# Kernel optimization log

Measured on AMD Instinct MI355X. Metric: run time of the kernel, lower is better.

Reference implementation:

```python
import jax, jax.numpy as jnp
import numpy as np

B, L, D, N = 1, 4096, 1536, 12
d = D // N            # head_dim = 128
c = d // 2            # rope channels per head = 64
EPS = 1e-6
MAX_POS = 1024


def setup_inputs() -> dict:
    key = jax.random.key(0)
    ks = jax.random.split(key, 8)
    s = 0.02
    # RoPE tables: freqs[m, j] = m * theta^{-j/c}; torch stores exp(i*ang) as complex64
    inv = 1.0 / (10000.0 ** (jnp.arange(c, dtype=jnp.float32) / c))
    ang = jnp.arange(MAX_POS, dtype=jnp.float32)[:, None] * inv[None, :]
    return {
        'x': jax.random.normal(ks[0], (B, L, D), jnp.float32),
        'seq_lens': jnp.array([L], jnp.int32),
        'grid_sizes': jnp.array([[4, 32, 32]], jnp.int32),  # f*h*w == L
        'freqs_cos': jnp.cos(ang),
        'freqs_sin': jnp.sin(ang),
        'Wq': jax.random.normal(ks[1], (D, D), jnp.float32) * s,
        'bq': jnp.zeros((D,), jnp.float32),
        'Wk': jax.random.normal(ks[2], (D, D), jnp.float32) * s,
        'bk': jnp.zeros((D,), jnp.float32),
        'Wv': jax.random.normal(ks[3], (D, D), jnp.float32) * s,
        'bv': jnp.zeros((D,), jnp.float32),
        'Wo': jax.random.normal(ks[4], (D, D), jnp.float32) * s,
        'bo': jnp.zeros((D,), jnp.float32),
        'gq': jnp.ones((D,), jnp.float32),
        'gk': jnp.ones((D,), jnp.float32),
    }


def rms_norm(x, g):
    # WanRMSNorm over the full model dim, computed in fp32
    v = jnp.mean(x.astype(jnp.float32) ** 2, axis=-1, keepdims=True)
    return (x * jax.lax.rsqrt(v + EPS)).astype(x.dtype) * g


def rope_apply(x4, grid_sizes, fcos, fsin):
    # x4: [B, L, N, d]; grid_sizes: [B, 3]; applies 3D (f,h,w) RoPE per batch
    gs = np.asarray(grid_sizes)  # concrete grid sizes (structural constants)
    c1 = c - 2 * (c // 3)
    c2 = c // 3
    outs = []
    for i in range(x4.shape[0]):
        f, h, w = (int(gs[i, 0]), int(gs[i, 1]), int(gs[i, 2]))
        sl = f * h * w

        def grid(tab):
            a = jnp.broadcast_to(tab[:f, None, None, :c1], (f, h, w, c1))
            b = jnp.broadcast_to(tab[None, :h, None, c1:c1 + c2], (f, h, w, c2))
            cc = jnp.broadcast_to(tab[None, None, :w, c1 + c2:c], (f, h, w, c2))
            return jnp.concatenate([a, b, cc], axis=-1).reshape(sl, 1, c)

        cos_i, sin_i = grid(fcos), grid(fsin)
        xi = x4[i, :sl]                    # [sl, N, d]
        xr, xim = xi[..., 0::2], xi[..., 1::2]  # complex pairs are interleaved
        o_re = xr * cos_i - xim * sin_i
        o_im = xr * sin_i + xim * cos_i
        rot = jnp.stack([o_re, o_im], axis=-1).reshape(sl, x4.shape[2], d)
        outs.append(jnp.concatenate([rot, x4[i, sl:]], axis=0))
    return jnp.stack(outs).astype(x4.dtype)


def reference(x, seq_lens, grid_sizes, freqs_cos, freqs_sin,
              Wq, bq, Wk, bk, Wv, bv, Wo, bo, gq, gk):
    q = rms_norm(x @ Wq.T + bq, gq).reshape(B, L, N, d)
    k = rms_norm(x @ Wk.T + bk, gk).reshape(B, L, N, d)
    v = (x @ Wv.T + bv).reshape(B, L, N, d)
    q = rope_apply(q, grid_sizes, freqs_cos, freqs_sin)
    k = rope_apply(k, grid_sizes, freqs_cos, freqs_sin)
    scale = 1.0 / jnp.sqrt(jnp.float32(d))
    scores = jnp.einsum('bqnd,bknd->bnqk', q, k) * scale
    kmask = jnp.arange(L)[None, :] < seq_lens[:, None]        # [B, L]
    scores = jnp.where(kmask[:, None, None, :], scores, jnp.float32(-1e30))
    p = jax.nn.softmax(scores, axis=-1)
    out = jnp.einsum('bnqk,bknd->bqnd', p, v).reshape(B, L, D)
    return out @ Wo.T + bo
```

## Files before the change

kernel.cpp:

```cpp
#include <hip/hip_runtime.h>

#define L_ 4096
#define D_ 1536
#define NH 12
#define HD 128

typedef __attribute__((ext_vector_type(8))) __bf16 bf16x8;
typedef __attribute__((ext_vector_type(8))) unsigned short ushort8v;
typedef __attribute__((ext_vector_type(4))) float floatx4;

#if __has_builtin(__builtin_amdgcn_exp2f)
#define EXP2F(x) __builtin_amdgcn_exp2f(x)
#else
#define EXP2F(x) exp2f(x)
#endif

__device__ __forceinline__ unsigned short f2bf(float f) {
  union { float f; unsigned int u; } v; v.f = f;
  unsigned int u = v.u;
  return (unsigned short)((u + 0x7fffu + ((u >> 16) & 1u)) >> 16);
}
__device__ __forceinline__ float bf2f(unsigned short h) {
  union { unsigned int u; float f; } v; v.u = ((unsigned int)h) << 16;
  return v.f;
}

__global__ __launch_bounds__(256) void cvt_f32_bf16(const float* __restrict__ in,
                                                    unsigned short* __restrict__ out,
                                                    int n8) {
  int i = blockIdx.x * 256 + threadIdx.x;
  if (i >= n8) return;
  const float4* p = (const float4*)(in + (size_t)i * 8);
  float4 a = p[0], b = p[1];
  ushort8v o;
  o[0] = f2bf(a.x); o[1] = f2bf(a.y); o[2] = f2bf(a.z); o[3] = f2bf(a.w);
  o[4] = f2bf(b.x); o[5] = f2bf(b.y); o[6] = f2bf(b.z); o[7] = f2bf(b.w);
  *(ushort8v*)(out + (size_t)i * 8) = o;
}

template <int MODE>
__device__ __forceinline__ void gemm_core(const unsigned short* __restrict__ A,
                                          const unsigned short* __restrict__ Bw,
                                          const float* __restrict__ bias,
                                          void* __restrict__ Cout,
                                          int M, int Nn, int K,
                                          int m0, int n0,
                                          unsigned short* As, unsigned short* Bs) {
  int t = threadIdx.x;
  int lane = t & 63, wv = t >> 6;
  int wm = (wv & 1) * 64, wn = (wv >> 1) * 64;
  floatx4 zero = {0.f, 0.f, 0.f, 0.f};
  floatx4 acc[4][4];
#pragma unroll
  for (int i = 0; i < 4; ++i)
#pragma unroll
    for (int j = 0; j < 4; ++j) acc[i][j] = zero;
  int fm = lane & 15, fk = (lane >> 4) * 8;

  for (int kt = 0; kt < K; kt += 32) {
    __syncthreads();
#pragma unroll
    for (int it = 0; it < 2; ++it) {
      int c = it * 256 + t;
      int row = c >> 2, col = (c & 3) * 8;
      const unsigned short* ga = A + (size_t)(m0 + row) * K + kt + col;
      const unsigned short* gb = Bw + (size_t)(n0 + row) * K + kt + col;
      __builtin_amdgcn_global_load_lds(
          (const __attribute__((address_space(1))) void*)ga,
          (__attribute__((address_space(3))) void*)((char*)As + (it * 256 + wv * 64) * 16),
          16, 0, 0);
      __builtin_amdgcn_global_load_lds(
          (const __attribute__((address_space(1))) void*)gb,
          (__attribute__((address_space(3))) void*)((char*)Bs + (it * 256 + wv * 64) * 16),
          16, 0, 0);
    }
    __syncthreads();
    bf16x8 af[4], bfr[4];
#pragma unroll
    for (int i = 0; i < 4; ++i) {
      af[i]  = *(const bf16x8*)&As[(wm + 16 * i + fm) * 32 + fk];
      bfr[i] = *(const bf16x8*)&Bs[(wn + 16 * i + fm) * 32 + fk];
    }
#pragma unroll
    for (int i = 0; i < 4; ++i)
#pragma unroll
      for (int j = 0; j < 4; ++j)
        acc[i][j] = __builtin_amdgcn_mfma_f32_16x16x32_bf16(af[i], bfr[j], acc[i][j], 0, 0, 0);
  }

  int fr = (lane >> 4) * 4;
#pragma unroll
  for (int j = 0; j < 4; ++j) {
    int col = n0 + wn + 16 * j + fm;
    float bz = bias[col];
#pragma unroll
    for (int i = 0; i < 4; ++i) {
      int row0 = m0 + wm + 16 * i + fr;
      if (MODE == 2) {
        ushort4 pk = make_ushort4(f2bf(acc[i][j][0] + bz), f2bf(acc[i][j][1] + bz),
                                  f2bf(acc[i][j][2] + bz), f2bf(acc[i][j][3] + bz));
        size_t off = (size_t)(row0 >> 5) * Nn * 32 + (size_t)col * 32 + (row0 & 31);
        *(ushort4*)&((unsigned short*)Cout)[off] = pk;
      } else {
#pragma unroll
        for (int r = 0; r < 4; ++r) {
          float val = acc[i][j][r] + bz;
          if (MODE == 1) ((unsigned short*)Cout)[(size_t)(row0 + r) * Nn + col] = f2bf(val);
          else           ((float*)Cout)[(size_t)(row0 + r) * Nn + col] = val;
        }
      }
    }
  }
}

template <int MODE>
__global__ __launch_bounds__(256) void gemm_bt(const unsigned short* __restrict__ A,
                                               const unsigned short* __restrict__ Bw,
                                               const float* __restrict__ bias,
                                               void* __restrict__ Cout,
                                               int M, int Nn, int K) {
  __shared__ unsigned short As[128 * 32];
  __shared__ unsigned short Bs[128 * 32];
  gemm_core<MODE>(A, Bw, bias, Cout, M, Nn, K, blockIdx.y * 128, blockIdx.x * 128, As, Bs);
}

__global__ __launch_bounds__(256) void gemm_qkv(const unsigned short* __restrict__ xb,
                                                const unsigned short* __restrict__ wq,
                                                const unsigned short* __restrict__ wk,
                                                const unsigned short* __restrict__ wv,
                                                const float* __restrict__ bq,
                                                const float* __restrict__ bk,
                                                const float* __restrict__ bv,
                                                unsigned short* __restrict__ outq,
                                                unsigned short* __restrict__ outk,
                                                unsigned short* __restrict__ outv) {
  __shared__ unsigned short As[128 * 32];
  __shared__ unsigned short Bs[128 * 32];
  int which = blockIdx.x / (D_ / 128);
  int n0 = (blockIdx.x % (D_ / 128)) * 128;
  int m0 = blockIdx.y * 128;
  if (which == 0)
    gemm_core<1>(xb, wq, bq, outq, L_, D_, D_, m0, n0, As, Bs);
  else if (which == 1)
    gemm_core<1>(xb, wk, bk, outk, L_, D_, D_, m0, n0, As, Bs);
  else
    gemm_core<2>(xb, wv, bv, outv, L_, D_, D_, m0, n0, As, Bs);
}

__global__ __launch_bounds__(256) void rmsrope(unsigned short* __restrict__ qb,
                                               unsigned short* __restrict__ kb,
                                               const float* __restrict__ gq,
                                               const float* __restrict__ gk,
                                               const float* __restrict__ fcos,
                                               const float* __restrict__ fsin,
                                               const int* __restrict__ grid_sizes) {
  int row = blockIdx.x;
  unsigned short* buf = (blockIdx.y == 0) ? qb : kb;
  const float* g = (blockIdx.y == 0) ? gq : gk;
  float osc = (blockIdx.y == 0) ? 0.1275174475f : 1.0f;
  int t = threadIdx.x;
  float xr[3], xi[3];
#pragma unroll
  for (int i = 0; i < 3; ++i) {
    int p = t + i * 256;
    unsigned int raw = *(const unsigned int*)&buf[(size_t)row * D_ + 2 * p];
    xr[i] = bf2f((unsigned short)(raw & 0xffffu));
    xi[i] = bf2f((unsigned short)(raw >> 16));
  }
  float ss = 0.f;
#pragma unroll
  for (int i = 0; i < 3; ++i) ss += xr[i] * xr[i] + xi[i] * xi[i];
  for (int off = 32; off > 0; off >>= 1) ss += __shfl_down(ss, off);
  __shared__ float red[4];
  if ((t & 63) == 0) red[t >> 6] = ss;
  __syncthreads();
  float rs = rsqrtf((red[0] + red[1] + red[2] + red[3]) * (1.0f / D_) + 1e-6f);

  int gf = grid_sizes[0], gh = grid_sizes[1], gw = grid_sizes[2];
  int sl = gf * gh * gw;
  int hw = gh * gw;
  int fi = row / hw, rem = row - fi * hw;
  int hi = rem / gw, wi = rem - hi * gw;
  bool dorope = row < sl;
#pragma unroll
  for (int i = 0; i < 3; ++i) {
    int p = t + i * 256;
    int j = p & 63;
    float a = xr[i] * rs * g[2 * p];
    float b = xi[i] * rs * g[2 * p + 1];
    if (dorope) {
      int pos = (j < 22) ? fi : ((j < 43) ? hi : wi);
      float cs = fcos[pos * 64 + j], sn = fsin[pos * 64 + j];
      float oa = a * cs - b * sn;
      float ob = a * sn + b * cs;
      a = oa; b = ob;
    }
    a *= osc; b *= osc;
    unsigned int packed = (unsigned int)f2bf(a) | ((unsigned int)f2bf(b) << 16);
    *(unsigned int*)&buf[(size_t)row * D_ + 2 * p] = packed;
  }
}

__global__ __launch_bounds__(256, 2) void attn7(const unsigned short* __restrict__ Qb,
                                                const unsigned short* __restrict__ Kb,
                                                const unsigned short* __restrict__ Vt,
                                                float* __restrict__ Op0,
                                                float* __restrict__ Op1,
                                                float* __restrict__ lp,
                                                const int* __restrict__ seq_lens) {
  __shared__ unsigned short Ks[2][4096];
  __shared__ unsigned short Vs[2][4096];
  int t = threadIdx.x, lane = t & 63, w = t >> 6;
  int id = blockIdx.x;
  int u2 = (id & 7) * 96 + (id >> 3);
  int half = u2 & 1, v = u2 >> 1;
  int h = v >> 5, qt = v & 31;
  int q0 = qt * 128 + w * 32;
  int kv0 = half * 2048;
  float* Opart = half ? Op1 : Op0;
  float* lpart = lp + (size_t)half * L_ * NH;
  int seqlen = seq_lens[0];
  int fl = lane & 15, fg = lane >> 4;

  bf16x8 qf[2][4];
#pragma unroll
  for (int nj = 0; nj < 2; ++nj)
#pragma unroll
    for (int kd = 0; kd < 4; ++kd)
      qf[nj][kd] = *(const bf16x8*)&Qb[((size_t)(q0 + nj * 16 + fl) * NH + h) * HD + kd * 32 + fg * 8];

  const unsigned short* kp[2];
  const unsigned short* vp[2];
#pragma unroll
  for (int i = 0; i < 2; ++i) {
    int c = t + i * 256;
    int dgroup = c >> 5, permrow = c & 31;
    int kd = dgroup >> 2, fgc = dgroup & 3, mi = permrow >> 4, flc = permrow & 15;
    int key = (((flc & 12) << 1) | (flc & 3)) + (mi << 2);
    kp[i] = Kb + ((size_t)(kv0 + key) * NH + h) * HD + kd * 32 + fgc * 8;
    int vd = c & 127, vkg = c >> 7;
    vp[i] = Vt + (size_t)(kv0 >> 5) * (D_ * 32) + ((size_t)(h * HD + vd)) * 32 + vkg * 8;
  }
  const int STEP = 32 * NH * HD;

  auto stage = [&](int b) {
#pragma unroll
    for (int i = 0; i < 2; ++i) {
      __builtin_amdgcn_global_load_lds(
          (const __attribute__((address_space(1))) void*)kp[i],
          (__attribute__((address_space(3))) void*)&Ks[b][(i * 256 + w * 64) * 8],
          16, 0, 0);
      __builtin_amdgcn_global_load_lds(
          (const __attribute__((address_space(1))) void*)vp[i],
          (__attribute__((address_space(3))) void*)&Vs[b][(i * 256 + w * 64) * 8],
          16, 0, 0);
      kp[i] += STEP; vp[i] += STEP;
    }
  };

  floatx4 o[2][8];
  floatx4 zero = {0.f, 0.f, 0.f, 0.f};
#pragma unroll
  for (int nj = 0; nj < 2; ++nj)
#pragma unroll
    for (int nt = 0; nt < 8; ++nt) o[nj][nt] = zero;
  float lr[2] = {0.f, 0.f};

  stage(0);
  for (int kt = 0; kt < 2048; kt += 32) {
    int cur = (kt >> 5) & 1;
    __syncthreads();
    if (kt + 32 < 2048) stage(cur ^ 1);

    floatx4 s[2][2];
    s[0][0] = zero; s[0][1] = zero; s[1][0] = zero; s[1][1] = zero;
#pragma unroll
    for (int kd = 0; kd < 4; ++kd)
#pragma unroll
      for (int mi = 0; mi < 2; ++mi) {
        bf16x8 kf = *(const bf16x8*)&Ks[cur][(((kd << 2) | fg) * 32 + (mi << 4) + fl) * 8];
#pragma unroll
        for (int nj = 0; nj < 2; ++nj)
          s[mi][nj] = __builtin_amdgcn_mfma_f32_16x16x32_bf16(kf, qf[nj][kd], s[mi][nj], 0, 0, 0);
      }

    bf16x8 pb[2];
    bool full = (kv0 + kt + 32 <= seqlen);
#pragma unroll
    for (int nj = 0; nj < 2; ++nj) {
      float pv[8];
      if (full) {
#pragma unroll
        for (int mi = 0; mi < 2; ++mi)
#pragma unroll
          for (int r = 0; r < 4; ++r) pv[mi * 4 + r] = EXP2F(s[mi][nj][r]);
      } else {
#pragma unroll
        for (int mi = 0; mi < 2; ++mi)
#pragma unroll
          for (int r = 0; r < 4; ++r) {
            int key = kv0 + kt + fg * 8 + mi * 4 + r;
            pv[mi * 4 + r] = (key < seqlen) ? EXP2F(s[mi][nj][r]) : 0.f;
          }
      }
      lr[nj] += ((pv[0] + pv[1]) + (pv[2] + pv[3])) + ((pv[4] + pv[5]) + (pv[6] + pv[7]));
      union { unsigned int u[4]; bf16x8 v; } pk;
#pragma unroll
      for (int jj = 0; jj < 4; ++jj) {
        unsigned int a = __builtin_bit_cast(unsigned int, pv[2 * jj]) + 0x8000u;
        unsigned int b = __builtin_bit_cast(unsigned int, pv[2 * jj + 1]) + 0x8000u;
        pk.u[jj] = (a >> 16) | (b & 0xffff0000u);
      }
      pb[nj] = pk.v;
    }

#pragma unroll
    for (int nt = 0; nt < 8; ++nt) {
      bf16x8 vf = *(const bf16x8*)&Vs[cur][((fg << 7) + (nt << 4) + fl) * 8];
#pragma unroll
      for (int nj = 0; nj < 2; ++nj)
        o[nj][nt] = __builtin_amdgcn_mfma_f32_16x16x32_bf16(pb[nj], vf, o[nj][nt], 0, 0, 0);
    }
  }

#pragma unroll
  for (int nj = 0; nj < 2; ++nj) {
    lr[nj] += __shfl_xor(lr[nj], 16);
    lr[nj] += __shfl_xor(lr[nj], 32);
    int rowb = q0 + nj * 16 + fg * 4;
#pragma unroll
    for (int nt = 0; nt < 8; ++nt) {
      int dcol = h * HD + nt * 16 + fl;
      Opart[(size_t)(rowb + 0) * D_ + dcol] = o[nj][nt][0];
      Opart[(size_t)(rowb + 1) * D_ + dcol] = o[nj][nt][1];
      Opart[(size_t)(rowb + 2) * D_ + dcol] = o[nj][nt][2];
      Opart[(size_t)(rowb + 3) * D_ + dcol] = o[nj][nt][3];
    }
    if (fg == 0) lpart[(size_t)(q0 + nj * 16 + fl) * NH + h] = lr[nj];
  }
}

__global__ __launch_bounds__(256) void attn_combine(const float* __restrict__ Op0,
                                                    const float* __restrict__ Op1,
                                                    const float* __restrict__ lp,
                                                    unsigned short* __restrict__ out) {
  int gid = blockIdx.x * 256 + threadIdx.x;
  int q = gid / (D_ / 8);
  int col = (gid - q * (D_ / 8)) * 8;
  int h = col >> 7;
  float l0 = lp[(size_t)q * NH + h];
  float l1 = lp[(size_t)L_ * NH + (size_t)q * NH + h];
  float inv = 1.0f / (l0 + l1);
  const float4* p0 = (const float4*)(Op0 + (size_t)q * D_ + col);
  const float4* p1 = (const float4*)(Op1 + (size_t)q * D_ + col);
  float4 a0 = p0[0], a1 = p0[1], b0 = p1[0], b1 = p1[1];
  ushort8v o;
  o[0] = f2bf((a0.x + b0.x) * inv); o[1] = f2bf((a0.y + b0.y) * inv);
  o[2] = f2bf((a0.z + b0.z) * inv); o[3] = f2bf((a0.w + b0.w) * inv);
  o[4] = f2bf((a1.x + b1.x) * inv); o[5] = f2bf((a1.y + b1.y) * inv);
  o[6] = f2bf((a1.z + b1.z) * inv); o[7] = f2bf((a1.w + b1.w) * inv);
  *(ushort8v*)(out + (size_t)q * D_ + col) = o;
}

__global__ __launch_bounds__(256, 2) void attn5(const unsigned short* __restrict__ Qb,
                                                const unsigned short* __restrict__ Kb,
                                                const unsigned short* __restrict__ Vt,
                                                unsigned short* __restrict__ Ob,
                                                const int* __restrict__ seq_lens) {
  __shared__ unsigned short Ks[2][4096];
  __shared__ unsigned short Vs[2][4096];
  int t = threadIdx.x, lane = t & 63, w = t >> 6;
  int id = blockIdx.x;
  int u = (id & 7) * 48 + (id >> 3);
  int h = u >> 5, qt = u & 31;
  int q0 = qt * 128 + w * 32;
  int seqlen = seq_lens[0];
  int fl = lane & 15, fg = lane >> 4;

  bf16x8 qf[2][4];
#pragma unroll
  for (int nj = 0; nj < 2; ++nj)
#pragma unroll
    for (int kd = 0; kd < 4; ++kd)
      qf[nj][kd] = *(const bf16x8*)&Qb[((size_t)(q0 + nj * 16 + fl) * NH + h) * HD + kd * 32 + fg * 8];

  const unsigned short* kp[2];
  const unsigned short* vp[2];
#pragma unroll
  for (int i = 0; i < 2; ++i) {
    int c = t + i * 256;
    int dgroup = c >> 5, permrow = c & 31;
    int kd = dgroup >> 2, fgc = dgroup & 3, mi = permrow >> 4, flc = permrow & 15;
    int key = (((flc & 12) << 1) | (flc & 3)) + (mi << 2);
    kp[i] = Kb + ((size_t)key * NH + h) * HD + kd * 32 + fgc * 8;
    int vd = c & 127, vkg = c >> 7;
    vp[i] = Vt + ((size_t)(h * HD + vd)) * 32 + vkg * 8;
  }
  const int STEP = 32 * NH * HD;

  auto stage = [&](int b) {
#pragma unroll
    for (int i = 0; i < 2; ++i) {
      __builtin_amdgcn_global_load_lds(
          (const __attribute__((address_space(1))) void*)kp[i],
          (__attribute__((address_space(3))) void*)&Ks[b][(i * 256 + w * 64) * 8],
          16, 0, 0);
      __builtin_amdgcn_global_load_lds(
          (const __attribute__((address_space(1))) void*)vp[i],
          (__attribute__((address_space(3))) void*)&Vs[b][(i * 256 + w * 64) * 8],
          16, 0, 0);
      kp[i] += STEP; vp[i] += STEP;
    }
  };

  floatx4 o[2][8];
  floatx4 zero = {0.f, 0.f, 0.f, 0.f};
#pragma unroll
  for (int nj = 0; nj < 2; ++nj)
#pragma unroll
    for (int nt = 0; nt < 8; ++nt) o[nj][nt] = zero;
  float lr[2] = {0.f, 0.f};

  stage(0);
  for (int kt = 0; kt < L_; kt += 32) {
    int cur = (kt >> 5) & 1;
    __syncthreads();
    if (kt + 32 < L_) stage(cur ^ 1);

    floatx4 s[2][2];
    s[0][0] = zero; s[0][1] = zero; s[1][0] = zero; s[1][1] = zero;
#pragma unroll
    for (int kd = 0; kd < 4; ++kd)
#pragma unroll
      for (int mi = 0; mi < 2; ++mi) {
        bf16x8 kf = *(const bf16x8*)&Ks[cur][(((kd << 2) | fg) * 32 + (mi << 4) + fl) * 8];
#pragma unroll
        for (int nj = 0; nj < 2; ++nj)
          s[mi][nj] = __builtin_amdgcn_mfma_f32_16x16x32_bf16(kf, qf[nj][kd], s[mi][nj], 0, 0, 0);
      }

    bf16x8 pb[2];
    bool full = (kt + 32 <= seqlen);
#pragma unroll
    for (int nj = 0; nj < 2; ++nj) {
      float pv[8];
      if (full) {
#pragma unroll
        for (int mi = 0; mi < 2; ++mi)
#pragma unroll
          for (int r = 0; r < 4; ++r) pv[mi * 4 + r] = EXP2F(s[mi][nj][r]);
      } else {
#pragma unroll
        for (int mi = 0; mi < 2; ++mi)
#pragma unroll
          for (int r = 0; r < 4; ++r) {
            int key = kt + fg * 8 + mi * 4 + r;
            pv[mi * 4 + r] = (key < seqlen) ? EXP2F(s[mi][nj][r]) : 0.f;
          }
      }
      lr[nj] += ((pv[0] + pv[1]) + (pv[2] + pv[3])) + ((pv[4] + pv[5]) + (pv[6] + pv[7]));
      union { unsigned int u[4]; bf16x8 v; } pk;
#pragma unroll
      for (int jj = 0; jj < 4; ++jj) {
        unsigned int a = __builtin_bit_cast(unsigned int, pv[2 * jj]) + 0x8000u;
        unsigned int b = __builtin_bit_cast(unsigned int, pv[2 * jj + 1]) + 0x8000u;
        pk.u[jj] = (a >> 16) | (b & 0xffff0000u);
      }
      pb[nj] = pk.v;
    }

#pragma unroll
    for (int nt = 0; nt < 8; ++nt) {
      bf16x8 vf = *(const bf16x8*)&Vs[cur][((fg << 7) + (nt << 4) + fl) * 8];
#pragma unroll
      for (int nj = 0; nj < 2; ++nj)
        o[nj][nt] = __builtin_amdgcn_mfma_f32_16x16x32_bf16(pb[nj], vf, o[nj][nt], 0, 0, 0);
    }
  }

#pragma unroll
  for (int nj = 0; nj < 2; ++nj) {
    lr[nj] += __shfl_xor(lr[nj], 16);
    lr[nj] += __shfl_xor(lr[nj], 32);
    float inv = 1.0f / lr[nj];
    int rowb = q0 + nj * 16 + fg * 4;
#pragma unroll
    for (int nt = 0; nt < 8; ++nt) {
      int dcol = h * HD + nt * 16 + fl;
      Ob[(size_t)(rowb + 0) * D_ + dcol] = f2bf(o[nj][nt][0] * inv);
      Ob[(size_t)(rowb + 1) * D_ + dcol] = f2bf(o[nj][nt][1] * inv);
      Ob[(size_t)(rowb + 2) * D_ + dcol] = f2bf(o[nj][nt][2] * inv);
      Ob[(size_t)(rowb + 3) * D_ + dcol] = f2bf(o[nj][nt][3] * inv);
    }
  }
}

extern "C" void kernel_launch(void* const* d_in, const int* in_sizes, int n_in,
                              void* d_out, int out_size, void* d_ws, size_t ws_size,
                              hipStream_t stream) {
  (void)in_sizes; (void)n_in; (void)out_size;
  const float* x    = (const float*)d_in[0];
  const int* seqln  = (const int*)d_in[1];
  const int* gsz    = (const int*)d_in[2];
  const float* fcos = (const float*)d_in[3];
  const float* fsin = (const float*)d_in[4];
  const float* Wq = (const float*)d_in[5];
  const float* bq = (const float*)d_in[6];
  const float* Wk = (const float*)d_in[7];
  const float* bk = (const float*)d_in[8];
  const float* Wv = (const float*)d_in[9];
  const float* bv = (const float*)d_in[10];
  const float* Wo = (const float*)d_in[11];
  const float* bo = (const float*)d_in[12];
  const float* gq = (const float*)d_in[13];
  const float* gk = (const float*)d_in[14];

  char* ws = (char*)d_ws;
  size_t LD2  = (size_t)L_ * D_ * 2;
  size_t WD2  = (size_t)D_ * D_ * 2;
  size_t LD4  = (size_t)L_ * D_ * 4;
  size_t LNH4 = (size_t)L_ * NH * 4;
  unsigned short* xb  = (unsigned short*)(ws);
  unsigned short* qb  = (unsigned short*)(ws + LD2);
  unsigned short* kb  = (unsigned short*)(ws + 2 * LD2);
  unsigned short* vtb = (unsigned short*)(ws + 3 * LD2);
  unsigned short* wb0 = (unsigned short*)(ws + 4 * LD2);
  unsigned short* ab  = xb;

  int nx8 = L_ * D_ / 8, nw8 = D_ * D_ / 8;
  dim3 gg(D_ / 128, L_ / 128);

  cvt_f32_bf16<<<(nx8 + 255) / 256, 256, 0, stream>>>(x, xb, nx8);

  bool fusedw = ws_size >= 4 * LD2 + 3 * WD2;
  if (fusedw) {
    unsigned short* wb1 = (unsigned short*)(ws + 4 * LD2 + WD2);
    unsigned short* wb2 = (unsigned short*)(ws + 4 * LD2 + 2 * WD2);
    cvt_f32_bf16<<<(nw8 + 255) / 256, 256, 0, stream>>>(Wq, wb0, nw8);
    cvt_f32_bf16<<<(nw8 + 255) / 256, 256, 0, stream>>>(Wk, wb1, nw8);
    cvt_f32_bf16<<<(nw8 + 255) / 256, 256, 0, stream>>>(Wv, wb2, nw8);
    gemm_qkv<<<dim3(3 * D_ / 128, L_ / 128), 256, 0, stream>>>(
        xb, wb0, wb1, wb2, bq, bk, bv, qb, kb, vtb);
  } else {
    cvt_f32_bf16<<<(nw8 + 255) / 256, 256, 0, stream>>>(Wq, wb0, nw8);
    gemm_bt<1><<<gg, 256, 0, stream>>>(xb, wb0, bq, qb, L_, D_, D_);
    cvt_f32_bf16<<<(nw8 + 255) / 256, 256, 0, stream>>>(Wk, wb0, nw8);
    gemm_bt<1><<<gg, 256, 0, stream>>>(xb, wb0, bk, kb, L_, D_, D_);
    cvt_f32_bf16<<<(nw8 + 255) / 256, 256, 0, stream>>>(Wv, wb0, nw8);
    gemm_bt<2><<<gg, 256, 0, stream>>>(xb, wb0, bv, vtb, L_, D_, D_);
  }

  rmsrope<<<dim3(L_, 2), 256, 0, stream>>>(qb, kb, gq, gk, fcos, fsin, gsz);

  size_t splitBase = 4 * LD2 + 3 * WD2;
  bool splitk = fusedw && (ws_size >= splitBase + LD4 + 2 * LNH4);
  if (splitk) {
    float* Op0 = (float*)d_out;
    float* Op1 = (float*)(ws + splitBase);
    float* lp  = (float*)(ws + splitBase + LD4);
    attn7<<<dim3(768), 256, 0, stream>>>(qb, kb, vtb, Op0, Op1, lp, seqln);
    attn_combine<<<dim3(L_ * D_ / 8 / 256), 256, 0, stream>>>(Op0, Op1, lp, ab);
  } else {
    attn5<<<dim3(384), 256, 0, stream>>>(qb, kb, vtb, ab, seqln);
  }

  cvt_f32_bf16<<<(nw8 + 255) / 256, 256, 0, stream>>>(Wo, wb0, nw8);
  gemm_bt<0><<<gg, 256, 0, stream>>>(ab, wb0, bo, d_out, L_, D_, D_);
}
```

Baseline: 404.8 us.

## Generalize split-KV attention to four key splits and fuse all f32-to-bf16 conversions

```diff
diff --git a/kernel.cpp b/kernel.cpp
--- a/kernel.cpp
+++ b/kernel.cpp
@@ -25,17 +25,41 @@
   return v.f;
 }
 
-__global__ __launch_bounds__(256) void cvt_f32_bf16(const float* __restrict__ in,
-                                                    unsigned short* __restrict__ out,
-                                                    int n8) {
-  int i = blockIdx.x * 256 + threadIdx.x;
-  if (i >= n8) return;
+__device__ __forceinline__ void cvt8(const float* __restrict__ in,
+                                     unsigned short* __restrict__ out, int i) {
   const float4* p = (const float4*)(in + (size_t)i * 8);
   float4 a = p[0], b = p[1];
   ushort8v o;
   o[0] = f2bf(a.x); o[1] = f2bf(a.y); o[2] = f2bf(a.z); o[3] = f2bf(a.w);
   o[4] = f2bf(b.x); o[5] = f2bf(b.y); o[6] = f2bf(b.z); o[7] = f2bf(b.w);
   *(ushort8v*)(out + (size_t)i * 8) = o;
+}
+
+__global__ __launch_bounds__(256) void cvt_f32_bf16(const float* __restrict__ in,
+                                                    unsigned short* __restrict__ out,
+                                                    int n8) {
+  int i = blockIdx.x * 256 + threadIdx.x;
+  if (i >= n8) return;
+  cvt8(in, out, i);
+}
+
+__global__ __launch_bounds__(256) void cvt_all(const float* __restrict__ x,
+                                               const float* __restrict__ wq,
+                                               const float* __restrict__ wk,
+                                               const float* __restrict__ wv,
+                                               const float* __restrict__ wo,
+                                               unsigned short* __restrict__ xb,
+                                               unsigned short* __restrict__ b0,
+                                               unsigned short* __restrict__ b1,
+                                               unsigned short* __restrict__ b2,
+                                               unsigned short* __restrict__ b3) {
+  const int NX = L_ * D_ / 8, NW = D_ * D_ / 8;
+  int i = blockIdx.x * 256 + threadIdx.x;
+  if (i < NX)               { cvt8(x,  xb, i); }
+  else if (i < NX + NW)     { cvt8(wq, b0, i - NX); }
+  else if (i < NX + 2 * NW) { cvt8(wk, b1, i - NX - NW); }
+  else if (i < NX + 3 * NW) { cvt8(wv, b2, i - NX - 2 * NW); }
+  else                      { cvt8(wo, b3, i - NX - 3 * NW); }
 }
 
 template <int MODE>
@@ -201,24 +225,26 @@
   }
 }
 
-__global__ __launch_bounds__(256, 2) void attn7(const unsigned short* __restrict__ Qb,
+template <int NS>
+__global__ __launch_bounds__(256, 2) void attnS(const unsigned short* __restrict__ Qb,
                                                 const unsigned short* __restrict__ Kb,
                                                 const unsigned short* __restrict__ Vt,
-                                                float* __restrict__ Op0,
-                                                float* __restrict__ Op1,
+                                                float* __restrict__ Opd,
+                                                float* __restrict__ Opw,
                                                 float* __restrict__ lp,
                                                 const int* __restrict__ seq_lens) {
   __shared__ unsigned short Ks[2][4096];
   __shared__ unsigned short Vs[2][4096];
+  const int KEYS = L_ / NS;
   int t = threadIdx.x, lane = t & 63, w = t >> 6;
   int id = blockIdx.x;
-  int u2 = (id & 7) * 96 + (id >> 3);
-  int half = u2 & 1, v = u2 >> 1;
+  int u2 = (id & 7) * (NS * 48) + (id >> 3);
+  int split = u2 % NS, v = u2 / NS;
   int h = v >> 5, qt = v & 31;
   int q0 = qt * 128 + w * 32;
-  int kv0 = half * 2048;
-  float* Opart = half ? Op1 : Op0;
-  float* lpart = lp + (size_t)half * L_ * NH;
+  int kv0 = split * KEYS;
+  float* Opart = (split == 0) ? Opd : (Opw + (size_t)(split - 1) * L_ * D_);
+  float* lpart = lp + (size_t)split * L_ * NH;
   int seqlen = seq_lens[0];
   int fl = lane & 15, fg = lane >> 4;
 
@@ -267,10 +293,10 @@
   float lr[2] = {0.f, 0.f};
 
   stage(0);
-  for (int kt = 0; kt < 2048; kt += 32) {
+  for (int kt = 0; kt < KEYS; kt += 32) {
     int cur = (kt >> 5) & 1;
     __syncthreads();
-    if (kt + 32 < 2048) stage(cur ^ 1);
+    if (kt + 32 < KEYS) stage(cur ^ 1);
 
     floatx4 s[2][2];
     s[0][0] = zero; s[0][1] = zero; s[1][0] = zero; s[1][1] = zero;
@@ -340,25 +366,36 @@
   }
 }
 
-__global__ __launch_bounds__(256) void attn_combine(const float* __restrict__ Op0,
-                                                    const float* __restrict__ Op1,
+template <int NS>
+__global__ __launch_bounds__(256) void attn_combine(const float* __restrict__ Opd,
+                                                    const float* __restrict__ Opw,
                                                     const float* __restrict__ lp,
                                                     unsigned short* __restrict__ out) {
   int gid = blockIdx.x * 256 + threadIdx.x;
   int q = gid / (D_ / 8);
   int col = (gid - q * (D_ / 8)) * 8;
   int h = col >> 7;
-  float l0 = lp[(size_t)q * NH + h];
-  float l1 = lp[(size_t)L_ * NH + (size_t)q * NH + h];
-  float inv = 1.0f / (l0 + l1);
-  const float4* p0 = (const float4*)(Op0 + (size_t)q * D_ + col);
-  const float4* p1 = (const float4*)(Op1 + (size_t)q * D_ + col);
-  float4 a0 = p0[0], a1 = p0[1], b0 = p1[0], b1 = p1[1];
+  float lsum = 0.f;
+#pragma unroll
+  for (int s = 0; s < NS; ++s) lsum += lp[(size_t)s * L_ * NH + (size_t)q * NH + h];
+  float inv = 1.0f / lsum;
+  float acc[8];
+  {
+    const float4* p = (const float4*)(Opd + (size_t)q * D_ + col);
+    float4 a = p[0], b = p[1];
+    acc[0] = a.x; acc[1] = a.y; acc[2] = a.z; acc[3] = a.w;
+    acc[4] = b.x; acc[5] = b.y; acc[6] = b.z; acc[7] = b.w;
+  }
+#pragma unroll
+  for (int s = 1; s < NS; ++s) {
+    const float4* p = (const float4*)(Opw + (size_t)(s - 1) * L_ * D_ + (size_t)q * D_ + col);
+    float4 a = p[0], b = p[1];
+    acc[0] += a.x; acc[1] += a.y; acc[2] += a.z; acc[3] += a.w;
+    acc[4] += b.x; acc[5] += b.y; acc[6] += b.z; acc[7] += b.w;
+  }
   ushort8v o;
-  o[0] = f2bf((a0.x + b0.x) * inv); o[1] = f2bf((a0.y + b0.y) * inv);
-  o[2] = f2bf((a0.z + b0.z) * inv); o[3] = f2bf((a0.w + b0.w) * inv);
-  o[4] = f2bf((a1.x + b1.x) * inv); o[5] = f2bf((a1.y + b1.y) * inv);
-  o[6] = f2bf((a1.z + b1.z) * inv); o[7] = f2bf((a1.w + b1.w) * inv);
+#pragma unroll
+  for (int e = 0; e < 8; ++e) o[e] = f2bf(acc[e] * inv);
   *(ushort8v*)(out + (size_t)q * D_ + col) = o;
 }
 
@@ -525,23 +562,26 @@
   unsigned short* kb  = (unsigned short*)(ws + 2 * LD2);
   unsigned short* vtb = (unsigned short*)(ws + 3 * LD2);
   unsigned short* wb0 = (unsigned short*)(ws + 4 * LD2);
+  unsigned short* wb1 = (unsigned short*)(ws + 4 * LD2 + WD2);
+  unsigned short* wb2 = (unsigned short*)(ws + 4 * LD2 + 2 * WD2);
+  unsigned short* wb3 = (unsigned short*)(ws + 4 * LD2 + 3 * WD2);
   unsigned short* ab  = xb;
 
   int nx8 = L_ * D_ / 8, nw8 = D_ * D_ / 8;
   dim3 gg(D_ / 128, L_ / 128);
 
-  cvt_f32_bf16<<<(nx8 + 255) / 256, 256, 0, stream>>>(x, xb, nx8);
-
-  bool fusedw = ws_size >= 4 * LD2 + 3 * WD2;
+  size_t base  = 4 * LD2 + 4 * WD2;
+  size_t need2 = base + LD4 + 2 * LNH4;
+  size_t need4 = base + 3 * LD4 + 4 * LNH4;
+  bool fusedw = ws_size >= base;
+
   if (fusedw) {
-    unsigned short* wb1 = (unsigned short*)(ws + 4 * LD2 + WD2);
-    unsigned short* wb2 = (unsigned short*)(ws + 4 * LD2 + 2 * WD2);
-    cvt_f32_bf16<<<(nw8 + 255) / 256, 256, 0, stream>>>(Wq, wb0, nw8);
-    cvt_f32_bf16<<<(nw8 + 255) / 256, 256, 0, stream>>>(Wk, wb1, nw8);
-    cvt_f32_bf16<<<(nw8 + 255) / 256, 256, 0, stream>>>(Wv, wb2, nw8);
+    int ntot = nx8 + 4 * nw8;
+    cvt_all<<<ntot / 256, 256, 0, stream>>>(x, Wq, Wk, Wv, Wo, xb, wb0, wb1, wb2, wb3);
     gemm_qkv<<<dim3(3 * D_ / 128, L_ / 128), 256, 0, stream>>>(
         xb, wb0, wb1, wb2, bq, bk, bv, qb, kb, vtb);
   } else {
+    cvt_f32_bf16<<<(nx8 + 255) / 256, 256, 0, stream>>>(x, xb, nx8);
     cvt_f32_bf16<<<(nw8 + 255) / 256, 256, 0, stream>>>(Wq, wb0, nw8);
     gemm_bt<1><<<gg, 256, 0, stream>>>(xb, wb0, bq, qb, L_, D_, D_);
     cvt_f32_bf16<<<(nw8 + 255) / 256, 256, 0, stream>>>(Wk, wb0, nw8);
@@ -552,18 +592,26 @@
 
   rmsrope<<<dim3(L_, 2), 256, 0, stream>>>(qb, kb, gq, gk, fcos, fsin, gsz);
 
-  size_t splitBase = 4 * LD2 + 3 * WD2;
-  bool splitk = fusedw && (ws_size >= splitBase + LD4 + 2 * LNH4);
-  if (splitk) {
-    float* Op0 = (float*)d_out;
-    float* Op1 = (float*)(ws + splitBase);
-    float* lp  = (float*)(ws + splitBase + LD4);
-    attn7<<<dim3(768), 256, 0, stream>>>(qb, kb, vtb, Op0, Op1, lp, seqln);
-    attn_combine<<<dim3(L_ * D_ / 8 / 256), 256, 0, stream>>>(Op0, Op1, lp, ab);
+  if (fusedw && ws_size >= need4) {
+    float* Opd = (float*)d_out;
+    float* Opw = (float*)(ws + base);
+    float* lp  = (float*)(ws + base + 3 * LD4);
+    attnS<4><<<dim3(4 * 384), 256, 0, stream>>>(qb, kb, vtb, Opd, Opw, lp, seqln);
+    attn_combine<4><<<dim3(L_ * D_ / 8 / 256), 256, 0, stream>>>(Opd, Opw, lp, ab);
+  } else if (fusedw && ws_size >= need2) {
+    float* Opd = (float*)d_out;
+    float* Opw = (float*)(ws + base);
+    float* lp  = (float*)(ws + base + LD4);
+    attnS<2><<<dim3(2 * 384), 256, 0, stream>>>(qb, kb, vtb, Opd, Opw, lp, seqln);
+    attn_combine<2><<<dim3(L_ * D_ / 8 / 256), 256, 0, stream>>>(Opd, Opw, lp, ab);
   } else {
     attn5<<<dim3(384), 256, 0, stream>>>(qb, kb, vtb, ab, seqln);
   }
 
-  cvt_f32_bf16<<<(nw8 + 255) / 256, 256, 0, stream>>>(Wo, wb0, nw8);
-  gemm_bt<0><<<gg, 256, 0, stream>>>(ab, wb0, bo, d_out, L_, D_, D_);
-}
+  if (fusedw) {
+    gemm_bt<0><<<gg, 256, 0, stream>>>(ab, wb3, bo, d_out, L_, D_, D_);
+  } else {
+    cvt_f32_bf16<<<(nw8 + 255) / 256, 256, 0, stream>>>(Wo, wb0, nw8);
+    gemm_bt<0><<<gg, 256, 0, stream>>>(ab, wb0, bo, d_out, L_, D_, D_);
+  }
+}
```

Result: no change. 405.7 us (+0.2%).
